# Performance work log

Measured on AMD Instinct MI355X. Metric: run time of the kernel, lower is better.

Reference implementation:

```python
import jax, jax.numpy as jnp
import numpy as np
from itertools import product

# problem dims
B, D = 2, 80            # batch, grid side -> 2*80^3 = 1.024M voxel slots
N = 200000
CIN, COUT = 32, 64
KV = 27                 # 3x3x3 kernel volume


def _build_rulebook():
    """Submanifold conv rulebook: in_idx[k, j] = input row whose coord equals
    coord_j + offset_k, or N (zero pad row) if that voxel is empty/out of grid."""
    rng = np.random.default_rng(0)
    total = B * D ** 3
    flat = rng.choice(total, size=N, replace=False)
    b, rem = flat // D ** 3, flat % D ** 3
    x, y, z = rem // (D * D), (rem // D) % D, rem % D
    lookup = np.full(total, N, dtype=np.int64)  # empty -> pad index N
    lookup[flat] = np.arange(N)
    rows = []
    for dx, dy, dz in product((-1, 0, 1), repeat=3):  # kernel offsets, dilation=1
        nx, ny, nz = x + dx, y + dy, z + dz
        valid = (0 <= nx) & (nx < D) & (0 <= ny) & (ny < D) & (0 <= nz) & (nz < D)
        nflat = ((b * D + nx) * D + ny) * D + nz
        rows.append(np.where(valid, lookup[np.clip(nflat, 0, total - 1)], N))
    return np.stack(rows).astype(np.int32)  # [KV, N]


def setup_inputs() -> dict:
    key = jax.random.key(0)
    k1, k2, k3 = jax.random.split(key, 3)
    stdv = 1.0 / float(np.sqrt(CIN * KV))  # matches reset_parameters
    feats = jax.random.normal(k1, (N, CIN), dtype=jnp.float32)
    weight = jax.random.uniform(k2, (KV, CIN, COUT), jnp.float32, -stdv, stdv)
    bias = jax.random.uniform(k3, (COUT,), jnp.float32, -stdv, stdv)
    in_idx = jnp.asarray(_build_rulebook())
    return {"feats": feats, "weight": weight, "bias": bias, "in_idx": in_idx}


def reference(feats, weight, bias, in_idx):
    # pad row N = zeros so missing neighbors contribute nothing
    feats_pad = jnp.concatenate(
        [feats, jnp.zeros((1, feats.shape[1]), feats.dtype)], axis=0)  # [N+1, Cin]

    def body(acc, kw):  # scan over the 27 kernel offsets: gather -> matmul -> accumulate
        idx_k, w_k = kw                       # [N] int32, [Cin, Cout]
        return acc + feats_pad[idx_k] @ w_k, None

    out0 = jnp.zeros((feats.shape[0], weight.shape[2]), feats.dtype)  # [N, Cout]
    out, _ = jax.lax.scan(body, out0, (in_idx, weight))
    return out + bias
```

## Files before the change

### kernel.cpp

```cpp
#include <hip/hip_runtime.h>
#include <cstddef>
#include <cstdint>

#define NROWS  200000
#define CIN    32
#define COUT   64
#define KV     27
#define NWAVES (NROWS / 64)

typedef __attribute__((ext_vector_type(8))) short  short8;
typedef __attribute__((ext_vector_type(4))) float  f32x4;

__device__ __forceinline__ unsigned short f2bf(float x) {
  unsigned u = __builtin_bit_cast(unsigned, x);
  u += 0x7FFFu + ((u >> 16) & 1u);
  return (unsigned short)(u >> 16);
}

__global__ void prep_weight_kernel(const float* __restrict__ w,
                                   short8* __restrict__ wsB) {
  int tid = blockIdx.x * blockDim.x + threadIdx.x;
  if (tid >= KV * 4 * 64) return;
  int lane = tid & 63;
  int t    = (tid >> 6) & 3;
  int k    = tid >> 8;
  int col  = t * 16 + (lane & 15);
  int kin0 = (lane >> 4) * 8;
  short8 v;
#pragma unroll
  for (int f = 0; f < 8; ++f)
    v[f] = (short)f2bf(w[((size_t)k * CIN + kin0 + f) * COUT + col]);
  wsB[tid] = v;
}

__global__ void prep_feats_kernel(const float* __restrict__ feats,
                                  short8* __restrict__ fb) {
  int i = blockIdx.x * blockDim.x + threadIdx.x;
  const int total8 = (NROWS + 1) * CIN / 8;
  if (i >= total8) return;
  short8 v = {0, 0, 0, 0, 0, 0, 0, 0};
  if (i < NROWS * CIN / 8) {
    const f32x4* p = (const f32x4*)feats + (size_t)i * 2;
    f32x4 a = p[0], b = p[1];
#pragma unroll
    for (int f = 0; f < 4; ++f) {
      v[f]     = (short)f2bf(a[f]);
      v[4 + f] = (short)f2bf(b[f]);
    }
  }
  fb[i] = v;
}

__global__ __launch_bounds__(256, 4)
void spconv_mfma_kernel(const unsigned short* __restrict__ featsbf,
                        const short8* __restrict__ wsB,
                        const float* __restrict__ bias,
                        const int* __restrict__ in_idx,
                        float* __restrict__ out) {
  __shared__ int sIdx[4][KV][64];

  const int tid  = threadIdx.x;
  const int lane = tid & 63;
  const int w    = tid >> 6;
  const int wid  = (int)blockIdx.x * 4 + w;
  if (wid >= NWAVES) return;
  const int row0 = wid << 6;

  {
    int tmp[KV];
#pragma unroll
    for (int k = 0; k < KV; ++k)
      tmp[k] = in_idx[(size_t)k * NROWS + row0 + lane];
#pragma unroll
    for (int k = 0; k < KV; ++k)
      sIdx[w][k][lane] = tmp[k];
  }

  const int c16  = lane & 15;
  const int kg   = lane >> 4;
  const int koff = kg * 8;

  f32x4 acc[4][4];
#pragma unroll
  for (int t = 0; t < 4; ++t) {
    float bv = bias[t * 16 + c16];
    f32x4 bvv = {bv, bv, bv, bv};
#pragma unroll
    for (int m = 0; m < 4; ++m) acc[m][t] = bvv;
  }

  const short8* bp = wsB + lane;

  int idxc[4], idxn[4];
#pragma unroll
  for (int m = 0; m < 4; ++m) idxc[m] = sIdx[w][0][m * 16 + c16];

  for (int k = 0; k < KV; ++k) {
    const int kn = (k + 1 < KV) ? k + 1 : KV - 1;
#pragma unroll
    for (int m = 0; m < 4; ++m) idxn[m] = sIdx[w][kn][m * 16 + c16];

    short8 bfr[4];
#pragma unroll
    for (int t = 0; t < 4; ++t) bfr[t] = bp[(k * 4 + t) * 64];

    short8 afr[4];
#pragma unroll
    for (int m = 0; m < 4; ++m)
      afr[m] = *(const short8*)(featsbf + (size_t)idxc[m] * CIN + koff);

#pragma unroll
    for (int m = 0; m < 4; ++m) {
      acc[m][0] = __builtin_amdgcn_mfma_f32_16x16x32_bf16(afr[m], bfr[0], acc[m][0], 0, 0, 0);
      acc[m][1] = __builtin_amdgcn_mfma_f32_16x16x32_bf16(afr[m], bfr[1], acc[m][1], 0, 0, 0);
      acc[m][2] = __builtin_amdgcn_mfma_f32_16x16x32_bf16(afr[m], bfr[2], acc[m][2], 0, 0, 0);
      acc[m][3] = __builtin_amdgcn_mfma_f32_16x16x32_bf16(afr[m], bfr[3], acc[m][3], 0, 0, 0);
    }

#pragma unroll
    for (int m = 0; m < 4; ++m) idxc[m] = idxn[m];
  }

#pragma unroll
  for (int m = 0; m < 4; ++m)
#pragma unroll
    for (int t = 0; t < 4; ++t)
#pragma unroll
      for (int r = 0; r < 4; ++r)
        out[(size_t)(row0 + m * 16 + kg * 4 + r) * COUT + t * 16 + c16] = acc[m][t][r];
}

__global__ void spconv_naive_kernel(const float* __restrict__ feats,
                                    const float* __restrict__ w,
                                    const float* __restrict__ bias,
                                    const int* __restrict__ in_idx,
                                    float* __restrict__ out) {
  int gid = blockIdx.x * blockDim.x + threadIdx.x;
  if (gid >= NROWS * COUT) return;
  int row = gid / COUT, co = gid % COUT;
  float acc = bias[co];
  for (int k = 0; k < KV; ++k) {
    int idx = in_idx[(size_t)k * NROWS + row];
    if (idx < NROWS) {
      const float* fr = feats + (size_t)idx * CIN;
      const float* wk = w + (size_t)k * CIN * COUT + co;
#pragma unroll
      for (int c = 0; c < CIN; ++c) acc += fr[c] * wk[(size_t)c * COUT];
    }
  }
  out[gid] = acc;
}

extern "C" void kernel_launch(void* const* d_in, const int* in_sizes, int n_in,
                              void* d_out, int out_size, void* d_ws, size_t ws_size,
                              hipStream_t stream) {
  const float* feats  = (const float*)d_in[0];
  const float* weight = (const float*)d_in[1];
  const float* bias   = (const float*)d_in[2];
  const int*   in_idx = (const int*)d_in[3];
  float*       out    = (float*)d_out;

  const size_t wsB_bytes = (size_t)KV * 4 * 64 * 16;
  const size_t fb_bytes  = (size_t)(NROWS + 1) * CIN * 2;
  short8*         wsB     = (short8*)d_ws;
  unsigned short* featsbf = (unsigned short*)((char*)d_ws + wsB_bytes);

  if (ws_size >= wsB_bytes + fb_bytes) {
    prep_weight_kernel<<<27, 256, 0, stream>>>(weight, wsB);
    prep_feats_kernel<<<((NROWS + 1) * CIN / 8 + 255) / 256, 256, 0, stream>>>(
        feats, (short8*)featsbf);
    const int blocks = (NWAVES + 3) / 4;
    spconv_mfma_kernel<<<blocks, 256, 0, stream>>>(
        featsbf, wsB, bias, in_idx, out);
  } else {
    spconv_naive_kernel<<<(NROWS * COUT + 255) / 256, 256, 0, stream>>>(
        feats, weight, bias, in_idx, out);
  }
}
```

Measured before the change: 58.16 us.

## Prefetch next offset's gathered features and remap blocks across XCDs

Software-pipelines the gather so that the feature rows for offset k+1 are loaded while the MFMAs for offset k run, with indices read two steps ahead from shared memory. Block IDs are remapped so that each XCD processes a contiguous range of rows, which should improve L2 locality for neighbour gathers. The launch-bounds occupancy hint drops from 4 to 3 to leave room for the extra prefetch registers. Costs are higher register pressure and possibly lower occupancy, and the remap hardcodes a 782-block, 8-XCD split.

```diff
diff --git a/kernel.cpp b/kernel.cpp
--- a/kernel.cpp
+++ b/kernel.cpp
@@ -51,7 +51,7 @@
   fb[i] = v;
 }
 
-__global__ __launch_bounds__(256, 4)
+__global__ __launch_bounds__(256, 3)
 void spconv_mfma_kernel(const unsigned short* __restrict__ featsbf,
                         const short8* __restrict__ wsB,
                         const float* __restrict__ bias,
@@ -59,10 +59,15 @@
                         float* __restrict__ out) {
   __shared__ int sIdx[4][KV][64];
 
+  const int bid  = blockIdx.x;
+  const int xcd  = bid & 7;
+  const int bi   = bid >> 3;
+  const int sbid = (xcd < 6) ? xcd * 98 + bi : 6 * 98 + (xcd - 6) * 97 + bi;
+
   const int tid  = threadIdx.x;
   const int lane = tid & 63;
   const int w    = tid >> 6;
-  const int wid  = (int)blockIdx.x * 4 + w;
+  const int wid  = sbid * 4 + w;
   if (wid >= NWAVES) return;
   const int row0 = wid << 6;
 
@@ -94,31 +99,41 @@
   int idxc[4], idxn[4];
 #pragma unroll
   for (int m = 0; m < 4; ++m) idxc[m] = sIdx[w][0][m * 16 + c16];
+#pragma unroll
+  for (int m = 0; m < 4; ++m) idxn[m] = sIdx[w][1][m * 16 + c16];
+
+  short8 af[4];
+#pragma unroll
+  for (int m = 0; m < 4; ++m)
+    af[m] = *(const short8*)(featsbf + (size_t)idxc[m] * CIN + koff);
 
   for (int k = 0; k < KV; ++k) {
-    const int kn = (k + 1 < KV) ? k + 1 : KV - 1;
-#pragma unroll
-    for (int m = 0; m < 4; ++m) idxn[m] = sIdx[w][kn][m * 16 + c16];
-
     short8 bfr[4];
 #pragma unroll
     for (int t = 0; t < 4; ++t) bfr[t] = bp[(k * 4 + t) * 64];
 
-    short8 afr[4];
+    short8 ag[4];
 #pragma unroll
     for (int m = 0; m < 4; ++m)
-      afr[m] = *(const short8*)(featsbf + (size_t)idxc[m] * CIN + koff);
+      ag[m] = *(const short8*)(featsbf + (size_t)idxn[m] * CIN + koff);
+
+    const int kn = (k + 2 < KV) ? k + 2 : KV - 1;
+    int idx2[4];
+#pragma unroll
+    for (int m = 0; m < 4; ++m) idx2[m] = sIdx[w][kn][m * 16 + c16];
 
 #pragma unroll
     for (int m = 0; m < 4; ++m) {
-      acc[m][0] = __builtin_amdgcn_mfma_f32_16x16x32_bf16(afr[m], bfr[0], acc[m][0], 0, 0, 0);
-      acc[m][1] = __builtin_amdgcn_mfma_f32_16x16x32_bf16(afr[m], bfr[1], acc[m][1], 0, 0, 0);
-      acc[m][2] = __builtin_amdgcn_mfma_f32_16x16x32_bf16(afr[m], bfr[2], acc[m][2], 0, 0, 0);
-      acc[m][3] = __builtin_amdgcn_mfma_f32_16x16x32_bf16(afr[m], bfr[3], acc[m][3], 0, 0, 0);
+      acc[m][0] = __builtin_amdgcn_mfma_f32_16x16x32_bf16(af[m], bfr[0], acc[m][0], 0, 0, 0);
+      acc[m][1] = __builtin_amdgcn_mfma_f32_16x16x32_bf16(af[m], bfr[1], acc[m][1], 0, 0, 0);
+      acc[m][2] = __builtin_amdgcn_mfma_f32_16x16x32_bf16(af[m], bfr[2], acc[m][2], 0, 0, 0);
+      acc[m][3] = __builtin_amdgcn_mfma_f32_16x16x32_bf16(af[m], bfr[3], acc[m][3], 0, 0, 0);
     }
 
 #pragma unroll
-    for (int m = 0; m < 4; ++m) idxc[m] = idxn[m];
+    for (int m = 0; m < 4; ++m) {
+      af[m] = ag[m]; idxc[m] = idxn[m]; idxn[m] = idx2[m];
+    }
   }
 
 #pragma unroll
```

Result: slower. 68.19 us (+17.3%).

## Widen per-wave tile to 128 rows and swap MFMA operands for vectorized stores

Applied to the files above, without the earlier changes.

Each wave now covers 128 output rows (8 M-subtiles) instead of 64, so every weight fragment loaded per kernel offset feeds twice as many MFMAs. The MFMA operands are swapped so each lane holds four consecutive output columns, which turns the epilogue into 16-byte vector stores and the bias init into vector loads. Blocks shrink to 2 waves, and bounds checks are added for the ragged last tile. The cost is a larger accumulator footprint (128 VGPRs of accumulators), which may reduce occupancy, and fewer waves to hide gather latency.

```diff
diff --git a/kernel.cpp b/kernel.cpp
--- a/kernel.cpp
+++ b/kernel.cpp
@@ -6,7 +6,8 @@
 #define CIN    32
 #define COUT   64
 #define KV     27
-#define NWAVES (NROWS / 64)
+#define MW     8
+#define NTILES ((NROWS + 127) / 128)
 
 typedef __attribute__((ext_vector_type(8))) short  short8;
 typedef __attribute__((ext_vector_type(4))) float  f32x4;
@@ -51,83 +52,90 @@
   fb[i] = v;
 }
 
-__global__ __launch_bounds__(256, 4)
+__global__ __launch_bounds__(128, 2)
 void spconv_mfma_kernel(const unsigned short* __restrict__ featsbf,
                         const short8* __restrict__ wsB,
                         const float* __restrict__ bias,
                         const int* __restrict__ in_idx,
                         float* __restrict__ out) {
-  __shared__ int sIdx[4][KV][64];
+  __shared__ int sIdx[2][KV][128];
 
   const int tid  = threadIdx.x;
   const int lane = tid & 63;
   const int w    = tid >> 6;
-  const int wid  = (int)blockIdx.x * 4 + w;
-  if (wid >= NWAVES) return;
-  const int row0 = wid << 6;
+  int wid = (int)blockIdx.x * 2 + w;
+  if (wid >= NTILES) return;
+  const int row0 = wid << 7;
 
   {
-    int tmp[KV];
 #pragma unroll
-    for (int k = 0; k < KV; ++k)
-      tmp[k] = in_idx[(size_t)k * NROWS + row0 + lane];
+    for (int h = 0; h < 2; ++h) {
+      const int r = h * 64 + lane;
+      const int row = row0 + r;
+      int tmp[KV];
 #pragma unroll
-    for (int k = 0; k < KV; ++k)
-      sIdx[w][k][lane] = tmp[k];
+      for (int k = 0; k < KV; ++k)
+        tmp[k] = (row < NROWS) ? in_idx[(size_t)k * NROWS + row] : NROWS;
+#pragma unroll
+      for (int k = 0; k < KV; ++k)
+        sIdx[w][k][r] = tmp[k];
+    }
   }
 
   const int c16  = lane & 15;
   const int kg   = lane >> 4;
   const int koff = kg * 8;
 
-  f32x4 acc[4][4];
+  f32x4 acc[MW][4];
 #pragma unroll
   for (int t = 0; t < 4; ++t) {
-    float bv = bias[t * 16 + c16];
-    f32x4 bvv = {bv, bv, bv, bv};
+    const f32x4 bv = *(const f32x4*)(bias + t * 16 + kg * 4);
 #pragma unroll
-    for (int m = 0; m < 4; ++m) acc[m][t] = bvv;
+    for (int m = 0; m < MW; ++m) acc[m][t] = bv;
   }
 
   const short8* bp = wsB + lane;
 
-  int idxc[4], idxn[4];
+  int idxc[MW], idxn[MW];
 #pragma unroll
-  for (int m = 0; m < 4; ++m) idxc[m] = sIdx[w][0][m * 16 + c16];
+  for (int m = 0; m < MW; ++m) idxc[m] = sIdx[w][0][m * 16 + c16];
 
   for (int k = 0; k < KV; ++k) {
     const int kn = (k + 1 < KV) ? k + 1 : KV - 1;
 #pragma unroll
-    for (int m = 0; m < 4; ++m) idxn[m] = sIdx[w][kn][m * 16 + c16];
+    for (int m = 0; m < MW; ++m) idxn[m] = sIdx[w][kn][m * 16 + c16];
 
     short8 bfr[4];
 #pragma unroll
     for (int t = 0; t < 4; ++t) bfr[t] = bp[(k * 4 + t) * 64];
 
-    short8 afr[4];
+    short8 afr[MW];
 #pragma unroll
-    for (int m = 0; m < 4; ++m)
+    for (int m = 0; m < MW; ++m)
       afr[m] = *(const short8*)(featsbf + (size_t)idxc[m] * CIN + koff);
 
 #pragma unroll
-    for (int m = 0; m < 4; ++m) {
-      acc[m][0] = __builtin_amdgcn_mfma_f32_16x16x32_bf16(afr[m], bfr[0], acc[m][0], 0, 0, 0);
-      acc[m][1] = __builtin_amdgcn_mfma_f32_16x16x32_bf16(afr[m], bfr[1], acc[m][1], 0, 0, 0);
-      acc[m][2] = __builtin_amdgcn_mfma_f32_16x16x32_bf16(afr[m], bfr[2], acc[m][2], 0, 0, 0);
-      acc[m][3] = __builtin_amdgcn_mfma_f32_16x16x32_bf16(afr[m], bfr[3], acc[m][3], 0, 0, 0);
+    for (int m = 0; m < MW; ++m) {
+      acc[m][0] = __builtin_amdgcn_mfma_f32_16x16x32_bf16(bfr[0], afr[m], acc[m][0], 0, 0, 0);
+      acc[m][1] = __builtin_amdgcn_mfma_f32_16x16x32_bf16(bfr[1], afr[m], acc[m][1], 0, 0, 0);
+      acc[m][2] = __builtin_amdgcn_mfma_f32_16x16x32_bf16(bfr[2], afr[m], acc[m][2], 0, 0, 0);
+      acc[m][3] = __builtin_amdgcn_mfma_f32_16x16x32_bf16(bfr[3], afr[m], acc[m][3], 0, 0, 0);
     }
 
 #pragma unroll
-    for (int m = 0; m < 4; ++m) idxc[m] = idxn[m];
+    for (int m = 0; m < MW; ++m) idxc[m] = idxn[m];
   }
 
 #pragma unroll
-  for (int m = 0; m < 4; ++m)
+  for (int m = 0; m < MW; ++m) {
+    const int row = row0 + m * 16 + c16;
+    if (row < NROWS) {
+      float* op = out + (size_t)row * COUT + kg * 4;
 #pragma unroll
-    for (int t = 0; t < 4; ++t)
-#pragma unroll
-      for (int r = 0; r < 4; ++r)
-        out[(size_t)(row0 + m * 16 + kg * 4 + r) * COUT + t * 16 + c16] = acc[m][t][r];
+      for (int t = 0; t < 4; ++t)
+        *(f32x4*)(op + t * 16) = acc[m][t];
+    }
+  }
 }
 
 __global__ void spconv_naive_kernel(const float* __restrict__ feats,
@@ -169,8 +177,8 @@
     prep_weight_kernel<<<27, 256, 0, stream>>>(weight, wsB);
     prep_feats_kernel<<<((NROWS + 1) * CIN / 8 + 255) / 256, 256, 0, stream>>>(
         feats, (short8*)featsbf);
-    const int blocks = (NWAVES + 3) / 4;
-    spconv_mfma_kernel<<<blocks, 256, 0, stream>>>(
+    const int blocks = (NTILES + 1) / 2;
+    spconv_mfma_kernel<<<blocks, 128, 0, stream>>>(
         featsbf, wsB, bias, in_idx, out);
   } else {
     spconv_naive_kernel<<<(NROWS * COUT + 255) / 256, 256, 0, stream>>>(
```

Measured after the change: 78.64 us. +35.2%, slower.

## Split kernel-offset loop across wave pairs with LDS reduction

Applied to the files above, without the earlier changes.

Each 64-row tile is now processed by two waves, one covering kernel offsets 0-13 and the other 14-26. The two partial accumulators are combined through shared memory, and each wave writes half of the output rows. This shortens each wave's serial gather-MFMA chain and doubles the number of waves in flight, which helps hide gather latency. The cost is an extra LDS reduction with two block barriers, and the index buffer now aliases the reduction buffer.

```diff
diff --git a/kernel.cpp b/kernel.cpp
--- a/kernel.cpp
+++ b/kernel.cpp
@@ -6,7 +6,9 @@
 #define CIN    32
 #define COUT   64
 #define KV     27
-#define NWAVES (NROWS / 64)
+#define NK0    14
+#define NK1    13
+#define NTILES (NROWS / 64)
 
 typedef __attribute__((ext_vector_type(8))) short  short8;
 typedef __attribute__((ext_vector_type(4))) float  f32x4;
@@ -57,23 +59,36 @@
                         const float* __restrict__ bias,
                         const int* __restrict__ in_idx,
                         float* __restrict__ out) {
-  __shared__ int sIdx[4][KV][64];
+  __shared__ f32x4 sRed[2][2][2][4][64];
+  int* sIdxAll = (int*)&sRed[0][0][0][0][0];
 
   const int tid  = threadIdx.x;
   const int lane = tid & 63;
   const int w    = tid >> 6;
-  const int wid  = (int)blockIdx.x * 4 + w;
-  if (wid >= NWAVES) return;
-  const int row0 = wid << 6;
-
-  {
-    int tmp[KV];
-#pragma unroll
-    for (int k = 0; k < KV; ++k)
+  const int pr   = w >> 1;
+  const int di   = w & 1;
+  int tile = (int)blockIdx.x * 2 + pr;
+  if (tile > NTILES - 1) tile = NTILES - 1;
+  const int row0 = tile << 6;
+  const int nk    = di ? NK1 : NK0;
+  const int kbase = di ? NK0 : 0;
+
+  int* sIdxW = sIdxAll + w * (NK0 * 64);
+
+  if (di == 0) {
+    int tmp[NK0];
+#pragma unroll
+    for (int k = 0; k < NK0; ++k)
       tmp[k] = in_idx[(size_t)k * NROWS + row0 + lane];
 #pragma unroll
-    for (int k = 0; k < KV; ++k)
-      sIdx[w][k][lane] = tmp[k];
+    for (int k = 0; k < NK0; ++k) sIdxW[k * 64 + lane] = tmp[k];
+  } else {
+    int tmp[NK1];
+#pragma unroll
+    for (int k = 0; k < NK1; ++k)
+      tmp[k] = in_idx[(size_t)(NK0 + k) * NROWS + row0 + lane];
+#pragma unroll
+    for (int k = 0; k < NK1; ++k) sIdxW[k * 64 + lane] = tmp[k];
   }
 
   const int c16  = lane & 15;
@@ -83,26 +98,26 @@
   f32x4 acc[4][4];
 #pragma unroll
   for (int t = 0; t < 4; ++t) {
-    float bv = bias[t * 16 + c16];
+    float bv = (di == 0) ? bias[t * 16 + c16] : 0.0f;
     f32x4 bvv = {bv, bv, bv, bv};
 #pragma unroll
     for (int m = 0; m < 4; ++m) acc[m][t] = bvv;
   }
 
-  const short8* bp = wsB + lane;
+  const short8* bp = wsB + (size_t)kbase * 256 + lane;
 
   int idxc[4], idxn[4];
 #pragma unroll
-  for (int m = 0; m < 4; ++m) idxc[m] = sIdx[w][0][m * 16 + c16];
-
-  for (int k = 0; k < KV; ++k) {
-    const int kn = (k + 1 < KV) ? k + 1 : KV - 1;
-#pragma unroll
-    for (int m = 0; m < 4; ++m) idxn[m] = sIdx[w][kn][m * 16 + c16];
+  for (int m = 0; m < 4; ++m) idxc[m] = sIdxW[m * 16 + c16];
+
+  for (int kk = 0; kk < nk; ++kk) {
+    const int knn = (kk + 1 < nk) ? kk + 1 : nk - 1;
+#pragma unroll
+    for (int m = 0; m < 4; ++m) idxn[m] = sIdxW[knn * 64 + m * 16 + c16];
 
     short8 bfr[4];
 #pragma unroll
-    for (int t = 0; t < 4; ++t) bfr[t] = bp[(k * 4 + t) * 64];
+    for (int t = 0; t < 4; ++t) bfr[t] = bp[(kk * 4 + t) * 64];
 
     short8 afr[4];
 #pragma unroll
@@ -121,13 +136,26 @@
     for (int m = 0; m < 4; ++m) idxc[m] = idxn[m];
   }
 
-#pragma unroll
-  for (int m = 0; m < 4; ++m)
+  __syncthreads();
+  const int mw0 = di ? 0 : 2;
+#pragma unroll
+  for (int j = 0; j < 2; ++j)
 #pragma unroll
     for (int t = 0; t < 4; ++t)
+      sRed[pr][di][j][t][lane] = acc[mw0 + j][t];
+  __syncthreads();
+
+  const int ms0 = di ? 2 : 0;
+#pragma unroll
+  for (int j = 0; j < 2; ++j) {
+#pragma unroll
+    for (int t = 0; t < 4; ++t) {
+      f32x4 s = acc[ms0 + j][t] + sRed[pr][1 - di][j][t][lane];
 #pragma unroll
       for (int r = 0; r < 4; ++r)
-        out[(size_t)(row0 + m * 16 + kg * 4 + r) * COUT + t * 16 + c16] = acc[m][t][r];
+        out[(size_t)(row0 + (ms0 + j) * 16 + kg * 4 + r) * COUT + t * 16 + c16] = s[r];
+    }
+  }
 }
 
 __global__ void spconv_naive_kernel(const float* __restrict__ feats,
@@ -169,7 +197,7 @@
     prep_weight_kernel<<<27, 256, 0, stream>>>(weight, wsB);
     prep_feats_kernel<<<((NROWS + 1) * CIN / 8 + 255) / 256, 256, 0, stream>>>(
         feats, (short8*)featsbf);
-    const int blocks = (NWAVES + 3) / 4;
+    const int blocks = (NTILES + 1) / 2;
     spconv_mfma_kernel<<<blocks, 256, 0, stream>>>(
         featsbf, wsB, bias, in_idx, out);
   } else {
```

After: 86.90 us. +49.4%, slower.
